# Kernel optimization log

Hardware: AMD Instinct MI355X
Metric: run time of the kernel (lower is better)

## Reference

```python
import jax, jax.numpy as jnp
import numpy as np

N_FILTER = 64
IMAGE_SIZE = 64
CHANNELS = 3
N_CALLS = 16  # n_calls * 16 with n_calls=1
EPS = 1e-5


def _sobel_kernels(c):
    kx = jnp.array([[-1., 0., 1.], [-2., 0., 2.], [-1., 0., 1.]], jnp.float32) / 8.0
    ky = kx.T
    # depthwise OIHW kernels: (C, 1, 3, 3)
    return jnp.tile(kx[None, None], (c, 1, 1, 1)), jnp.tile(ky[None, None], (c, 1, 1, 1))


def _dwconv(x, k):
    return jax.lax.conv_general_dilated(
        x, k, window_strides=(1, 1), padding='SAME',
        feature_group_count=x.shape[1],
        dimension_numbers=('NCHW', 'OIHW', 'NCHW'))


def setup_inputs() -> dict:
    key = jax.random.key(0)
    k1, k2, k3 = jax.random.split(key, 3)
    B, L = 16, 512
    fin, fout = N_FILTER * 3, N_FILTER
    return {
        'lat': jax.random.normal(k1, (B, L), jnp.float32),
        'Wk': jax.random.normal(k2, (L, fin * fout), jnp.float32) * 0.02,
        'bk': jnp.zeros((fin * fout,), jnp.float32),
        'Wb': jax.random.normal(k3, (L, fout), jnp.float32) * 0.02,
        'bb': jnp.zeros((fout,), jnp.float32),
        'leak_factor': jnp.asarray(0.1, jnp.float32),
    }


def reference(lat, Wk, bk, Wb, bb, leak_factor):
    B = lat.shape[0]
    fin, fout = N_FILTER * 3, N_FILTER
    kx, ky = _sobel_kernels(N_FILTER)

    # seed: zeros with a 1.0 in channel 0 at the image center
    out0 = jnp.zeros((B, N_FILTER, IMAGE_SIZE, IMAGE_SIZE), jnp.float32)
    out0 = out0.at[:, 0, IMAGE_SIZE // 2, IMAGE_SIZE // 2].set(1.0)

    leak = jnp.clip(leak_factor, 0.001, 1000.0)

    # per-sample dynamic 1x1 conv weights/bias (constant across the loop)
    w = (lat @ Wk + bk).reshape(B, fout, fin)   # (B, fout, fin)
    b = (lat @ Wb + bb)                          # (B, fout)

    def step(out, _):
        # Sobel perception: [identity, grad_x, grad_y] -> (B, 3*nf, H, W)
        p = jnp.concatenate([out, _dwconv(out, kx), _dwconv(out, ky)], axis=1)
        # InstanceNorm2d (affine=False): normalize over H, W per sample/channel
        mu = p.mean(axis=(2, 3), keepdims=True)
        var = p.var(axis=(2, 3), keepdims=True)
        p = (p - mu) * jax.lax.rsqrt(var + EPS)
        # latent-conditioned dynamic 1x1 conv
        new = jnp.einsum('bchw,boc->bohw', p, w) + b[:, :, None, None]
        out = out + leak * new
        return out, out

    out, embs = jax.lax.scan(step, out0, None, length=N_CALLS)
    out_embs = jnp.concatenate([out0[None], embs], axis=0)  # (N_CALLS+1, B, nf, H, W)

    out_raw = out[:, :CHANNELS]
    return jnp.clip(out_raw, -1.0, 1.0), out_embs, out_raw
```

## Files before the change

kernel.cpp:

```cpp
#include <hip/hip_runtime.h>
#include <cstdint>
#include <cstddef>

#define NB 16
#define NC 64
#define HW 4096
#define SLICE ((size_t)(NB*NC*HW))
#define NSTEP 16

#define WS_WT    ((size_t)0)
#define WS_BV    ((size_t)196608)
#define WS_SV    ((size_t)197632)
#define WS_SVMU  ((size_t)200704)
#define WS_PLA   ((size_t)203776)
#define WS_PLB   ((size_t)4398080)

typedef _Float16 half8 __attribute__((ext_vector_type(8)));
typedef float f32x4 __attribute__((ext_vector_type(4)));

__global__ __launch_bounds__(256) void k_w(const float* __restrict__ lat,
    const float* __restrict__ Wk, const float* __restrict__ bk,
    const float* __restrict__ Wb, const float* __restrict__ bb,
    float* __restrict__ wT, float* __restrict__ bvec) {
  int t = threadIdx.x;
  if (blockIdx.x < 48) {
    int j = blockIdx.x*256 + t;
    float acc[16];
#pragma unroll
    for (int b = 0; b < 16; b++) acc[b] = 0.f;
#pragma unroll 4
    for (int k = 0; k < 512; k++) {
      float wv = Wk[(size_t)k*12288 + j];
#pragma unroll
      for (int b = 0; b < 16; b++) acc[b] = fmaf(lat[b*512 + k], wv, acc[b]);
    }
    int o = j / 192, cf = j % 192;
    int g = cf >> 6, c = cf & 63;
    float bkj = bk[j];
#pragma unroll
    for (int b = 0; b < 16; b++)
      wT[(((size_t)(b*3 + g))*64 + o)*64 + c] = acc[b] + bkj;
  } else if (t < 64) {
    int j = t;
    float acc[16];
#pragma unroll
    for (int b = 0; b < 16; b++) acc[b] = 0.f;
    for (int k = 0; k < 512; k++) {
      float wv = Wb[k*64 + j];
#pragma unroll
      for (int b = 0; b < 16; b++) acc[b] = fmaf(lat[b*512 + k], wv, acc[b]);
    }
    float bbj = bb[j];
#pragma unroll
    for (int b = 0; b < 16; b++) bvec[b*64 + j] = acc[b] + bbj;
  }
}

__global__ void k_init(float* __restrict__ e0, float* __restrict__ plA) {
  int f4 = blockIdx.x*256 + threadIdx.x;
  float4 v = make_float4(0.f, 0.f, 0.f, 0.f);
  if (f4 < 1048576) {
    if ((f4 & 65535) == 520) v.x = 1.0f;
    *(float4*)(e0 + (size_t)f4*4) = v;
  } else {
    int g4 = f4 - 1048576;
    if ((g4 & 65535) == 2080)
      v.x = __uint_as_float(0x00003C00u);
    *(float4*)(plA + (size_t)g4*4) = v;
  }
}

__global__ __launch_bounds__(256) void k_stats(const float* __restrict__ st,
    float* __restrict__ svb, float* __restrict__ svmub) {
  int c = blockIdx.x, b = blockIdx.y, t = threadIdx.x;
  __shared__ float red[4][6];
  const float* base = st + (size_t)(b*NC + c) * HW;
  int w = t & 63, wv = t >> 6, h0 = wv * 16;
  float x[18];
#pragma unroll
  for (int i = 0; i < 18; i++) {
    int row = h0 - 1 + i;
    x[i] = (row >= 0 && row < 64) ? base[row*64 + w] : 0.f;
  }
  float d[18], s[18];
#pragma unroll
  for (int i = 0; i < 18; i++) {
    float xl = __shfl(x[i], (w + 63) & 63);
    float xr = __shfl(x[i], (w + 1) & 63);
    if (w == 0)  xl = 0.f;
    if (w == 63) xr = 0.f;
    d[i] = xr - xl; s[i] = xl + 2.f*x[i] + xr;
  }
  float s0=0,q0=0,s1=0,q1=0,s2=0,q2=0;
#pragma unroll
  for (int k = 0; k < 16; k++) {
    float v  = x[k+1];
    float gx = (d[k] + 2.f*d[k+1] + d[k+2]) * 0.125f;
    float gy = (s[k+2] - s[k]) * 0.125f;
    s0 += v;  q0 = fmaf(v, v, q0);
    s1 += gx; q1 = fmaf(gx, gx, q1);
    s2 += gy; q2 = fmaf(gy, gy, q2);
  }
#pragma unroll
  for (int off = 32; off >= 1; off >>= 1) {
    s0 += __shfl_xor(s0, off); q0 += __shfl_xor(q0, off);
    s1 += __shfl_xor(s1, off); q1 += __shfl_xor(q1, off);
    s2 += __shfl_xor(s2, off); q2 += __shfl_xor(q2, off);
  }
  int lane = t & 63;
  if (lane == 0) {
    red[wv][0]=s0; red[wv][1]=q0; red[wv][2]=s1;
    red[wv][3]=q1; red[wv][4]=s2; red[wv][5]=q2;
  }
  __syncthreads();
  if (t == 0) {
    float r[6];
#pragma unroll
    for (int u = 0; u < 6; u++) r[u] = red[0][u]+red[1][u]+red[2][u]+red[3][u];
#pragma unroll
    for (int g = 0; g < 3; g++) {
      float mu  = r[2*g] * (1.f/HW);
      float var = fmaxf(r[2*g+1]*(1.f/HW) - mu*mu, 0.f);
      float sv  = 1.f / sqrtf(var + 1e-5f);
      svb  [b*192 + g*64 + c] = sv;
      svmub[b*192 + g*64 + c] = sv * mu;
    }
  }
}

struct SG {
  alignas(16) _Float16 Bwin[32768];
  float biasL[64];
};

__global__ __launch_bounds__(256, 2) void k_gemm(const float* __restrict__ st,
    float* __restrict__ stn, const float* __restrict__ wT,
    const float* __restrict__ bvec, const float* __restrict__ svb,
    const float* __restrict__ svmub, const _Float16* __restrict__ plR,
    _Float16* __restrict__ plW, const float* __restrict__ leakp,
    float* __restrict__ out0, float* __restrict__ out2, int last) {
  __shared__ SG sh;
  int bid = blockIdx.x, t = threadIdx.x;
  int b = bid >> 5;
  int r0 = ((((bid & 7) << 2) | ((bid >> 3) & 3))) << 1;
  int lane = t & 63, wt = t >> 6, c4 = lane >> 4;
  float leak = fminf(fmaxf(leakp[0], 0.001f), 1000.f);

  const _Float16* plb = plR + (size_t)b*524288;
#pragma unroll
  for (int i = 0; i < 16; i++) {
    int u = t + i*256;
    int pl = u >> 11, rest = u & 2047;
    int pxg = (r0 - 1)*64 + (rest & 255);
    int pxc = pxg < 0 ? 0 : (pxg > 4095 ? 4095 : pxg);
    const _Float16* gp = plb + ((size_t)pl*8 + (rest >> 8))*32768 + (size_t)pxc*8;
    float4 v = *(const float4*)gp;
    if (pxg < 0 || pxg > 4095) v = make_float4(0.f,0.f,0.f,0.f);
    *(float4*)(sh.Bwin + (size_t)u*8) = v;
  }

  int oa = wt*16 + (lane & 15);
  half8 whi[3][2], wlo[3][2];
  float biasacc = 0.f;
#pragma unroll
  for (int g = 0; g < 3; g++) {
#pragma unroll
    for (int kc = 0; kc < 2; kc++) {
      const float* wrow = wT + (((size_t)(b*3 + g))*64 + oa)*64 + kc*32 + c4*8;
      const float* svp  = svb   + b*192 + g*64 + kc*32 + c4*8;
      const float* svmp = svmub + b*192 + g*64 + kc*32 + c4*8;
      float4 wa = *(const float4*)wrow;  float4 wb2 = *(const float4*)(wrow + 4);
      float4 sa = *(const float4*)svp;   float4 sb2 = *(const float4*)(svp + 4);
      float4 ma = *(const float4*)svmp;  float4 mb2 = *(const float4*)(svmp + 4);
      float wv[8] = {wa.x,wa.y,wa.z,wa.w, wb2.x,wb2.y,wb2.z,wb2.w};
      float sv[8] = {sa.x,sa.y,sa.z,sa.w, sb2.x,sb2.y,sb2.z,sb2.w};
      float mv[8] = {ma.x,ma.y,ma.z,ma.w, mb2.x,mb2.y,mb2.z,mb2.w};
      half8 hv, lv;
#pragma unroll
      for (int jj = 0; jj < 8; jj++) {
        float scaled = wv[jj] * sv[jj];
        biasacc = fmaf(wv[jj], mv[jj], biasacc);
        _Float16 h = (_Float16)scaled;
        hv[jj] = h;
        lv[jj] = (_Float16)(scaled - (float)h);
      }
      whi[g][kc] = hv; wlo[g][kc] = lv;
    }
  }
  biasacc += __shfl_xor(biasacc, 16);
  biasacc += __shfl_xor(biasacc, 32);
  if (c4 == 0) sh.biasL[oa] = bvec[b*64 + oa] - biasacc;
  __syncthreads();

#pragma unroll
  for (int rr = 0; rr < 2; rr++) {
    int r = r0 + rr;
    f32x4 accA[4] = {}; f32x4 accB[12] = {}; f32x4 accC[12] = {};
#pragma unroll
    for (int kc = 0; kc < 2; kc++) {
#pragma unroll
      for (int n = 0; n < 12; n++) {
        int pxl = rr*64 + n*16 + (lane & 15);
        half8 bh = *(const half8*)(sh.Bwin + ((size_t)(     kc*4 + c4)*256 + pxl)*8);
        half8 bl = *(const half8*)(sh.Bwin + ((size_t)(8 +  kc*4 + c4)*256 + pxl)*8);
        accB[n] = __builtin_amdgcn_mfma_f32_16x16x32_f16(whi[1][kc], bh, accB[n], 0,0,0);
        accB[n] = __builtin_amdgcn_mfma_f32_16x16x32_f16(whi[1][kc], bl, accB[n], 0,0,0);
        accB[n] = __builtin_amdgcn_mfma_f32_16x16x32_f16(wlo[1][kc], bh, accB[n], 0,0,0);
        accC[n] = __builtin_amdgcn_mfma_f32_16x16x32_f16(whi[2][kc], bh, accC[n], 0,0,0);
        accC[n] = __builtin_amdgcn_mfma_f32_16x16x32_f16(whi[2][kc], bl, accC[n], 0,0,0);
        accC[n] = __builtin_amdgcn_mfma_f32_16x16x32_f16(wlo[2][kc], bh, accC[n], 0,0,0);
        if (n >= 4 && n < 8) {
          accA[n-4] = __builtin_amdgcn_mfma_f32_16x16x32_f16(whi[0][kc], bh, accA[n-4], 0,0,0);
          accA[n-4] = __builtin_amdgcn_mfma_f32_16x16x32_f16(whi[0][kc], bl, accA[n-4], 0,0,0);
          accA[n-4] = __builtin_amdgcn_mfma_f32_16x16x32_f16(wlo[0][kc], bh, accA[n-4], 0,0,0);
        }
      }
    }

    float nv16[16];
#pragma unroll
    for (int j = 0; j < 4; j++) {
      int o = wt*16 + (c4 << 2) + j;
      float Sx[4], Sy[4];
#pragma unroll
      for (int nc = 0; nc < 4; nc++) {
        Sx[nc] = accB[nc][j] + 2.f*accB[4+nc][j] + accB[8+nc][j];
        Sy[nc] = accC[8+nc][j] - accC[nc][j];
      }
      float bt = sh.biasL[o];
#pragma unroll
      for (int nc = 0; nc < 4; nc++) {
        int nm = (nc > 0) ? nc-1 : 0;
        int np = (nc < 3) ? nc+1 : 3;
        float xl1 = __shfl(Sx[nc], (lane - 1) & 63);
        float xl2 = (nc > 0) ? __shfl(Sx[nm], (lane + 15) & 63) : 0.f;
        float xL  = (lane & 15) ? xl1 : xl2;
        float xr1 = __shfl(Sx[nc], (lane + 1) & 63);
        float xr2 = (nc < 3) ? __shfl(Sx[np], (lane - 15) & 63) : 0.f;
        float xR  = ((lane & 15) == 15) ? xr2 : xr1;
        float yl1 = __shfl(Sy[nc], (lane - 1) & 63);
        float yl2 = (nc > 0) ? __shfl(Sy[nm], (lane + 15) & 63) : 0.f;
        float yL  = (lane & 15) ? yl1 : yl2;
        float yr1 = __shfl(Sy[nc], (lane + 1) & 63);
        float yr2 = (nc < 3) ? __shfl(Sy[np], (lane - 15) & 63) : 0.f;
        float yR  = ((lane & 15) == 15) ? yr2 : yr1;
        float gx = (xR - xL) * 0.125f;
        float gy = (yL + 2.f*Sy[nc] + yR) * 0.125f;
        float nw = accA[nc][j] + gx + gy + bt;
        int wpx = nc*16 + (lane & 15);
        size_t gi = (size_t)(b*NC + o)*HW + (size_t)r*64 + wpx;
        float nvv = st[gi] + leak * nw;
        stn[gi] = nvv;
        nv16[j*4 + nc] = nvv;
        if (last && o < 3) {
          size_t oi = (size_t)(b*3 + o)*HW + (size_t)r*64 + wpx;
          out2[oi] = nvv;
          out0[oi] = fminf(fmaxf(nvv, -1.f), 1.f);
        }
      }
    }

    if (!last) {
      int pl = c4 & 1;
      int g8 = wt*2 + (c4 >> 1);
      _Float16* pw = plW + (size_t)b*524288 + ((size_t)pl*8 + g8)*32768;
#pragma unroll
      for (int nc = 0; nc < 4; nc++) {
        float own[4], rcv[4];
#pragma unroll
        for (int j = 0; j < 4; j++) {
          own[j] = nv16[j*4 + nc];
          rcv[j] = __shfl_xor(own[j], 16);
        }
        float xx[8];
#pragma unroll
        for (int jj = 0; jj < 8; jj++)
          xx[jj] = ((jj >> 2) == (c4 & 1)) ? own[jj & 3] : rcv[jj & 3];
        half8 v8;
        if (pl == 0) {
#pragma unroll
          for (int jj = 0; jj < 8; jj++) v8[jj] = (_Float16)xx[jj];
        } else {
#pragma unroll
          for (int jj = 0; jj < 8; jj++) {
            _Float16 h = (_Float16)xx[jj];
            v8[jj] = (_Float16)(xx[jj] - (float)h);
          }
        }
        int gpx = r*64 + nc*16 + (lane & 15);
        *(half8*)(pw + (size_t)gpx*8) = v8;
      }
    }
  }
}

extern "C" void kernel_launch(void* const* d_in, const int* in_sizes, int n_in,
                              void* d_out, int out_size, void* d_ws, size_t ws_size,
                              hipStream_t stream) {
  const float* lat   = (const float*)d_in[0];
  const float* Wk    = (const float*)d_in[1];
  const float* bk    = (const float*)d_in[2];
  const float* Wb    = (const float*)d_in[3];
  const float* bb    = (const float*)d_in[4];
  const float* leakp = (const float*)d_in[5];
  float* out = (float*)d_out;
  float* ws  = (float*)d_ws;
  float* wT    = ws + WS_WT;
  float* bvec  = ws + WS_BV;
  float* svbuf = ws + WS_SV;
  float* svmub = ws + WS_SVMU;
  _Float16* plbuf[2] = { (_Float16*)(ws + WS_PLA), (_Float16*)(ws + WS_PLB) };
  float* out0 = out;
  float* embs = out + 196608;
  float* out2 = out + 196608 + 17*SLICE;

  hipLaunchKernelGGL(k_w,    dim3(49),   dim3(256), 0, stream, lat, Wk, bk, Wb, bb, wT, bvec);
  hipLaunchKernelGGL(k_init, dim3(8192), dim3(256), 0, stream, embs, ws + WS_PLA);
  for (int tstep = 0; tstep < NSTEP; tstep++) {
    const float* stc = embs + (size_t)tstep*SLICE;
    float*       stn = embs + (size_t)(tstep+1)*SLICE;
    hipLaunchKernelGGL(k_stats, dim3(64,16), dim3(256), 0, stream, stc, svbuf, svmub);
    hipLaunchKernelGGL(k_gemm, dim3(512), dim3(256), 0, stream,
                       stc, stn, wT, bvec, svbuf, svmub,
                       plbuf[tstep & 1], plbuf[(tstep+1) & 1], leakp,
                       out0, out2, (int)(tstep == NSTEP-1));
  }
}
```

Baseline: 600.4 us.

## Fuse instance-norm statistics into step kernel via halo recompute and atomics

Removes the separate per-step statistics kernel: each step kernel now recomputes one halo row above and below its two output rows so it can compute Sobel gradients of the new state and accumulate sum and sum-of-squares per channel with atomics into a triple-buffered stats array. The next step turns these sums into scale and shift in shared memory. This saves 16 kernel launches and a full re-read of the state each step. In exchange it doubles the MFMA work per block (4 rows instead of 2), enlarges shared memory, drops to one block per CU, and adds atomic contention.

```diff
diff --git a/kernel.cpp b/kernel.cpp
--- a/kernel.cpp
+++ b/kernel.cpp
@@ -10,10 +10,9 @@
 
 #define WS_WT    ((size_t)0)
 #define WS_BV    ((size_t)196608)
-#define WS_SV    ((size_t)197632)
-#define WS_SVMU  ((size_t)200704)
-#define WS_PLA   ((size_t)203776)
-#define WS_PLB   ((size_t)4398080)
+#define WS_STATS ((size_t)197632)
+#define WS_PLA   ((size_t)216064)
+#define WS_PLB   ((size_t)4410368)
 
 typedef _Float16 half8 __attribute__((ext_vector_type(8)));
 typedef float f32x4 __attribute__((ext_vector_type(4)));
@@ -56,8 +55,21 @@
   }
 }
 
-__global__ void k_init(float* __restrict__ e0, float* __restrict__ plA) {
-  int f4 = blockIdx.x*256 + threadIdx.x;
+__global__ void k_init(float* __restrict__ e0, float* __restrict__ plA,
+                       float* __restrict__ sb0, float* __restrict__ sb1) {
+  int t = threadIdx.x;
+  if (blockIdx.x == 0) {
+    for (int i = t; i < 6144; i += 256) {
+      int rem = i % 384;
+      int gc = rem >> 1, e = rem & 1;
+      float v = 0.f;
+      if (gc == 0) v = 1.0f;
+      else if ((gc == 64 || gc == 128) && e == 1) v = 0.1875f;
+      sb0[i] = v;
+      sb1[i] = 0.f;
+    }
+  }
+  int f4 = blockIdx.x*256 + t;
   float4 v = make_float4(0.f, 0.f, 0.f, 0.f);
   if (f4 < 1048576) {
     if ((f4 & 65535) == 520) v.x = 1.0f;
@@ -70,94 +82,48 @@
   }
 }
 
-__global__ __launch_bounds__(256) void k_stats(const float* __restrict__ st,
-    float* __restrict__ svb, float* __restrict__ svmub) {
-  int c = blockIdx.x, b = blockIdx.y, t = threadIdx.x;
-  __shared__ float red[4][6];
-  const float* base = st + (size_t)(b*NC + c) * HW;
-  int w = t & 63, wv = t >> 6, h0 = wv * 16;
-  float x[18];
-#pragma unroll
-  for (int i = 0; i < 18; i++) {
-    int row = h0 - 1 + i;
-    x[i] = (row >= 0 && row < 64) ? base[row*64 + w] : 0.f;
-  }
-  float d[18], s[18];
-#pragma unroll
-  for (int i = 0; i < 18; i++) {
-    float xl = __shfl(x[i], (w + 63) & 63);
-    float xr = __shfl(x[i], (w + 1) & 63);
-    if (w == 0)  xl = 0.f;
-    if (w == 63) xr = 0.f;
-    d[i] = xr - xl; s[i] = xl + 2.f*x[i] + xr;
-  }
-  float s0=0,q0=0,s1=0,q1=0,s2=0,q2=0;
-#pragma unroll
-  for (int k = 0; k < 16; k++) {
-    float v  = x[k+1];
-    float gx = (d[k] + 2.f*d[k+1] + d[k+2]) * 0.125f;
-    float gy = (s[k+2] - s[k]) * 0.125f;
-    s0 += v;  q0 = fmaf(v, v, q0);
-    s1 += gx; q1 = fmaf(gx, gx, q1);
-    s2 += gy; q2 = fmaf(gy, gy, q2);
-  }
-#pragma unroll
-  for (int off = 32; off >= 1; off >>= 1) {
-    s0 += __shfl_xor(s0, off); q0 += __shfl_xor(q0, off);
-    s1 += __shfl_xor(s1, off); q1 += __shfl_xor(q1, off);
-    s2 += __shfl_xor(s2, off); q2 += __shfl_xor(q2, off);
-  }
-  int lane = t & 63;
-  if (lane == 0) {
-    red[wv][0]=s0; red[wv][1]=q0; red[wv][2]=s1;
-    red[wv][3]=q1; red[wv][4]=s2; red[wv][5]=q2;
-  }
-  __syncthreads();
-  if (t == 0) {
-    float r[6];
-#pragma unroll
-    for (int u = 0; u < 6; u++) r[u] = red[0][u]+red[1][u]+red[2][u]+red[3][u];
-#pragma unroll
-    for (int g = 0; g < 3; g++) {
-      float mu  = r[2*g] * (1.f/HW);
-      float var = fmaxf(r[2*g+1]*(1.f/HW) - mu*mu, 0.f);
-      float sv  = 1.f / sqrtf(var + 1e-5f);
-      svb  [b*192 + g*64 + c] = sv;
-      svmub[b*192 + g*64 + c] = sv * mu;
-    }
-  }
-}
-
-struct SG {
-  alignas(16) _Float16 Bwin[32768];
-  float biasL[64];
+struct SG2 {
+  alignas(16) _Float16 Bwin[16*384*8];
+  float svL[192], svmuL[192], biasL[64];
 };
 
-__global__ __launch_bounds__(256, 2) void k_gemm(const float* __restrict__ st,
+__global__ __launch_bounds__(256, 1) void k_step(const float* __restrict__ st,
     float* __restrict__ stn, const float* __restrict__ wT,
-    const float* __restrict__ bvec, const float* __restrict__ svb,
-    const float* __restrict__ svmub, const _Float16* __restrict__ plR,
-    _Float16* __restrict__ plW, const float* __restrict__ leakp,
+    const float* __restrict__ bvec, const float* __restrict__ statsR,
+    float* __restrict__ statsW, float* __restrict__ statsZ,
+    const _Float16* __restrict__ plR, _Float16* __restrict__ plW,
+    const float* __restrict__ leakp,
     float* __restrict__ out0, float* __restrict__ out2, int last) {
-  __shared__ SG sh;
+  __shared__ SG2 sh;
   int bid = blockIdx.x, t = threadIdx.x;
   int b = bid >> 5;
   int r0 = ((((bid & 7) << 2) | ((bid >> 3) & 3))) << 1;
   int lane = t & 63, wt = t >> 6, c4 = lane >> 4;
   float leak = fminf(fmaxf(leakp[0], 0.001f), 1000.f);
 
+  if (t < 12) statsZ[bid*12 + t] = 0.f;
+
   const _Float16* plb = plR + (size_t)b*524288;
 #pragma unroll
-  for (int i = 0; i < 16; i++) {
+  for (int i = 0; i < 24; i++) {
     int u = t + i*256;
-    int pl = u >> 11, rest = u & 2047;
-    int pxg = (r0 - 1)*64 + (rest & 255);
+    int p = u / 384, wpx = u % 384;
+    int pxg = (r0 - 2)*64 + wpx;
     int pxc = pxg < 0 ? 0 : (pxg > 4095 ? 4095 : pxg);
-    const _Float16* gp = plb + ((size_t)pl*8 + (rest >> 8))*32768 + (size_t)pxc*8;
-    float4 v = *(const float4*)gp;
+    float4 v = *(const float4*)(plb + ((size_t)p*4096 + pxc)*8);
     if (pxg < 0 || pxg > 4095) v = make_float4(0.f,0.f,0.f,0.f);
-    *(float4*)(sh.Bwin + (size_t)u*8) = v;
-  }
+    *(float4*)(sh.Bwin + ((size_t)p*384 + wpx)*8) = v;
+  }
+
+  if (t < 192) {
+    float s = statsR[(b*192 + t)*2];
+    float q = statsR[(b*192 + t)*2 + 1];
+    float mu = s * (1.f/HW);
+    float var = fmaxf(q*(1.f/HW) - mu*mu, 0.f);
+    float sv = 1.f / sqrtf(var + 1e-5f);
+    sh.svL[t] = sv; sh.svmuL[t] = sv * mu;
+  }
+  __syncthreads();
 
   int oa = wt*16 + (lane & 15);
   half8 whi[3][2], wlo[3][2];
@@ -167,19 +133,14 @@
 #pragma unroll
     for (int kc = 0; kc < 2; kc++) {
       const float* wrow = wT + (((size_t)(b*3 + g))*64 + oa)*64 + kc*32 + c4*8;
-      const float* svp  = svb   + b*192 + g*64 + kc*32 + c4*8;
-      const float* svmp = svmub + b*192 + g*64 + kc*32 + c4*8;
       float4 wa = *(const float4*)wrow;  float4 wb2 = *(const float4*)(wrow + 4);
-      float4 sa = *(const float4*)svp;   float4 sb2 = *(const float4*)(svp + 4);
-      float4 ma = *(const float4*)svmp;  float4 mb2 = *(const float4*)(svmp + 4);
       float wv[8] = {wa.x,wa.y,wa.z,wa.w, wb2.x,wb2.y,wb2.z,wb2.w};
-      float sv[8] = {sa.x,sa.y,sa.z,sa.w, sb2.x,sb2.y,sb2.z,sb2.w};
-      float mv[8] = {ma.x,ma.y,ma.z,ma.w, mb2.x,mb2.y,mb2.z,mb2.w};
       half8 hv, lv;
 #pragma unroll
       for (int jj = 0; jj < 8; jj++) {
-        float scaled = wv[jj] * sv[jj];
-        biasacc = fmaf(wv[jj], mv[jj], biasacc);
+        int cg = g*64 + kc*32 + c4*8 + jj;
+        float scaled = wv[jj] * sh.svL[cg];
+        biasacc = fmaf(wv[jj], sh.svmuL[cg], biasacc);
         _Float16 h = (_Float16)scaled;
         hv[jj] = h;
         lv[jj] = (_Float16)(scaled - (float)h);
@@ -192,75 +153,87 @@
   if (c4 == 0) sh.biasL[oa] = bvec[b*64 + oa] - biasacc;
   __syncthreads();
 
-#pragma unroll
-  for (int rr = 0; rr < 2; rr++) {
-    int r = r0 + rr;
-    f32x4 accA[4] = {}; f32x4 accB[12] = {}; f32x4 accC[12] = {};
-#pragma unroll
-    for (int kc = 0; kc < 2; kc++) {
-#pragma unroll
-      for (int n = 0; n < 12; n++) {
-        int pxl = rr*64 + n*16 + (lane & 15);
-        half8 bh = *(const half8*)(sh.Bwin + ((size_t)(     kc*4 + c4)*256 + pxl)*8);
-        half8 bl = *(const half8*)(sh.Bwin + ((size_t)(8 +  kc*4 + c4)*256 + pxl)*8);
-        accB[n] = __builtin_amdgcn_mfma_f32_16x16x32_f16(whi[1][kc], bh, accB[n], 0,0,0);
-        accB[n] = __builtin_amdgcn_mfma_f32_16x16x32_f16(whi[1][kc], bl, accB[n], 0,0,0);
-        accB[n] = __builtin_amdgcn_mfma_f32_16x16x32_f16(wlo[1][kc], bh, accB[n], 0,0,0);
-        accC[n] = __builtin_amdgcn_mfma_f32_16x16x32_f16(whi[2][kc], bh, accC[n], 0,0,0);
-        accC[n] = __builtin_amdgcn_mfma_f32_16x16x32_f16(whi[2][kc], bl, accC[n], 0,0,0);
-        accC[n] = __builtin_amdgcn_mfma_f32_16x16x32_f16(wlo[2][kc], bh, accC[n], 0,0,0);
-        if (n >= 4 && n < 8) {
-          accA[n-4] = __builtin_amdgcn_mfma_f32_16x16x32_f16(whi[0][kc], bh, accA[n-4], 0,0,0);
-          accA[n-4] = __builtin_amdgcn_mfma_f32_16x16x32_f16(whi[0][kc], bl, accA[n-4], 0,0,0);
-          accA[n-4] = __builtin_amdgcn_mfma_f32_16x16x32_f16(wlo[0][kc], bh, accA[n-4], 0,0,0);
-        }
-      }
-    }
-
-    float nv16[16];
-#pragma unroll
-    for (int j = 0; j < 4; j++) {
-      int o = wt*16 + (c4 << 2) + j;
-      float Sx[4], Sy[4];
-#pragma unroll
-      for (int nc = 0; nc < 4; nc++) {
-        Sx[nc] = accB[nc][j] + 2.f*accB[4+nc][j] + accB[8+nc][j];
-        Sy[nc] = accC[8+nc][j] - accC[nc][j];
-      }
-      float bt = sh.biasL[o];
-#pragma unroll
-      for (int nc = 0; nc < 4; nc++) {
-        int nm = (nc > 0) ? nc-1 : 0;
-        int np = (nc < 3) ? nc+1 : 3;
-        float xl1 = __shfl(Sx[nc], (lane - 1) & 63);
-        float xl2 = (nc > 0) ? __shfl(Sx[nm], (lane + 15) & 63) : 0.f;
-        float xL  = (lane & 15) ? xl1 : xl2;
-        float xr1 = __shfl(Sx[nc], (lane + 1) & 63);
-        float xr2 = (nc < 3) ? __shfl(Sx[np], (lane - 15) & 63) : 0.f;
-        float xR  = ((lane & 15) == 15) ? xr2 : xr1;
-        float yl1 = __shfl(Sy[nc], (lane - 1) & 63);
-        float yl2 = (nc > 0) ? __shfl(Sy[nm], (lane + 15) & 63) : 0.f;
-        float yL  = (lane & 15) ? yl1 : yl2;
-        float yr1 = __shfl(Sy[nc], (lane + 1) & 63);
-        float yr2 = (nc < 3) ? __shfl(Sy[np], (lane - 15) & 63) : 0.f;
-        float yR  = ((lane & 15) == 15) ? yr2 : yr1;
-        float gx = (xR - xL) * 0.125f;
-        float gy = (yL + 2.f*Sy[nc] + yR) * 0.125f;
-        float nw = accA[nc][j] + gx + gy + bt;
-        int wpx = nc*16 + (lane & 15);
-        size_t gi = (size_t)(b*NC + o)*HW + (size_t)r*64 + wpx;
-        float nvv = st[gi] + leak * nw;
-        stn[gi] = nvv;
-        nv16[j*4 + nc] = nvv;
-        if (last && o < 3) {
-          size_t oi = (size_t)(b*3 + o)*HW + (size_t)r*64 + wpx;
-          out2[oi] = nvv;
-          out0[oi] = fminf(fmaxf(nvv, -1.f), 1.f);
-        }
-      }
-    }
-
-    if (!last) {
+  float nv4[4][16];
+
+#pragma unroll
+  for (int rr = 0; rr < 4; rr++) {
+    int r = r0 - 1 + rr;
+    if (r >= 0 && r < 64) {
+      f32x4 accA[4] = {}; f32x4 accB[12] = {}; f32x4 accC[12] = {};
+#pragma unroll
+      for (int kc = 0; kc < 2; kc++) {
+#pragma unroll
+        for (int n = 0; n < 12; n++) {
+          int pxl = rr*64 + n*16 + (lane & 15);
+          half8 bh = *(const half8*)(sh.Bwin + ((size_t)((     kc*4 + c4)*384) + pxl)*8);
+          half8 bl = *(const half8*)(sh.Bwin + ((size_t)((8 +  kc*4 + c4)*384) + pxl)*8);
+          accB[n] = __builtin_amdgcn_mfma_f32_16x16x32_f16(whi[1][kc], bh, accB[n], 0,0,0);
+          accB[n] = __builtin_amdgcn_mfma_f32_16x16x32_f16(whi[1][kc], bl, accB[n], 0,0,0);
+          accB[n] = __builtin_amdgcn_mfma_f32_16x16x32_f16(wlo[1][kc], bh, accB[n], 0,0,0);
+          accC[n] = __builtin_amdgcn_mfma_f32_16x16x32_f16(whi[2][kc], bh, accC[n], 0,0,0);
+          accC[n] = __builtin_amdgcn_mfma_f32_16x16x32_f16(whi[2][kc], bl, accC[n], 0,0,0);
+          accC[n] = __builtin_amdgcn_mfma_f32_16x16x32_f16(wlo[2][kc], bh, accC[n], 0,0,0);
+          if (n >= 4 && n < 8) {
+            accA[n-4] = __builtin_amdgcn_mfma_f32_16x16x32_f16(whi[0][kc], bh, accA[n-4], 0,0,0);
+            accA[n-4] = __builtin_amdgcn_mfma_f32_16x16x32_f16(whi[0][kc], bl, accA[n-4], 0,0,0);
+            accA[n-4] = __builtin_amdgcn_mfma_f32_16x16x32_f16(wlo[0][kc], bh, accA[n-4], 0,0,0);
+          }
+        }
+      }
+
+#pragma unroll
+      for (int j = 0; j < 4; j++) {
+        int o = wt*16 + (c4 << 2) + j;
+        float Sx[4], Sy[4];
+#pragma unroll
+        for (int nc = 0; nc < 4; nc++) {
+          Sx[nc] = accB[nc][j] + 2.f*accB[4+nc][j] + accB[8+nc][j];
+          Sy[nc] = accC[8+nc][j] - accC[nc][j];
+        }
+        float bt = sh.biasL[o];
+#pragma unroll
+        for (int nc = 0; nc < 4; nc++) {
+          int nm = (nc > 0) ? nc-1 : 0;
+          int np = (nc < 3) ? nc+1 : 3;
+          float xl1 = __shfl(Sx[nc], (lane - 1) & 63);
+          float xl2 = (nc > 0) ? __shfl(Sx[nm], (lane + 15) & 63) : 0.f;
+          float xL  = (lane & 15) ? xl1 : xl2;
+          float xr1 = __shfl(Sx[nc], (lane + 1) & 63);
+          float xr2 = (nc < 3) ? __shfl(Sx[np], (lane - 15) & 63) : 0.f;
+          float xR  = ((lane & 15) == 15) ? xr2 : xr1;
+          float yl1 = __shfl(Sy[nc], (lane - 1) & 63);
+          float yl2 = (nc > 0) ? __shfl(Sy[nm], (lane + 15) & 63) : 0.f;
+          float yL  = (lane & 15) ? yl1 : yl2;
+          float yr1 = __shfl(Sy[nc], (lane + 1) & 63);
+          float yr2 = (nc < 3) ? __shfl(Sy[np], (lane - 15) & 63) : 0.f;
+          float yR  = ((lane & 15) == 15) ? yr2 : yr1;
+          float gx = (xR - xL) * 0.125f;
+          float gy = (yL + 2.f*Sy[nc] + yR) * 0.125f;
+          float nw = accA[nc][j] + gx + gy + bt;
+          int wpx = nc*16 + (lane & 15);
+          size_t gi = (size_t)(b*NC + o)*HW + (size_t)r*64 + wpx;
+          float nvv = st[gi] + leak * nw;
+          nv4[rr][j*4 + nc] = nvv;
+          if (rr == 1 || rr == 2) {
+            stn[gi] = nvv;
+            if (last && o < 3) {
+              size_t oi = (size_t)(b*3 + o)*HW + (size_t)r*64 + wpx;
+              out2[oi] = nvv;
+              out0[oi] = fminf(fmaxf(nvv, -1.f), 1.f);
+            }
+          }
+        }
+      }
+    } else {
+#pragma unroll
+      for (int u = 0; u < 16; u++) nv4[rr][u] = 0.f;
+    }
+  }
+
+  if (!last) {
+#pragma unroll
+    for (int rr = 1; rr <= 2; rr++) {
+      int r = r0 - 1 + rr;
       int pl = c4 & 1;
       int g8 = wt*2 + (c4 >> 1);
       _Float16* pw = plW + (size_t)b*524288 + ((size_t)pl*8 + g8)*32768;
@@ -269,7 +242,7 @@
         float own[4], rcv[4];
 #pragma unroll
         for (int j = 0; j < 4; j++) {
-          own[j] = nv16[j*4 + nc];
+          own[j] = nv4[rr][j*4 + nc];
           rcv[j] = __shfl_xor(own[j], 16);
         }
         float xx[8];
@@ -289,6 +262,58 @@
         }
         int gpx = r*64 + nc*16 + (lane & 15);
         *(half8*)(pw + (size_t)gpx*8) = v8;
+      }
+    }
+
+#pragma unroll
+    for (int j = 0; j < 4; j++) {
+      float dxv[4][4], sxv[4][4];
+#pragma unroll
+      for (int rw = 0; rw < 4; rw++) {
+        float vv[4];
+#pragma unroll
+        for (int nc = 0; nc < 4; nc++) vv[nc] = nv4[rw][j*4 + nc];
+#pragma unroll
+        for (int nc = 0; nc < 4; nc++) {
+          int nm = (nc > 0) ? nc-1 : 0;
+          int np = (nc < 3) ? nc+1 : 3;
+          float xl1 = __shfl(vv[nc], (lane - 1) & 63);
+          float xl2 = (nc > 0) ? __shfl(vv[nm], (lane + 15) & 63) : 0.f;
+          float xL  = (lane & 15) ? xl1 : xl2;
+          float xr1 = __shfl(vv[nc], (lane + 1) & 63);
+          float xr2 = (nc < 3) ? __shfl(vv[np], (lane - 15) & 63) : 0.f;
+          float xR  = ((lane & 15) == 15) ? xr2 : xr1;
+          dxv[rw][nc] = xR - xL;
+          sxv[rw][nc] = xL + 2.f*vv[nc] + xR;
+        }
+      }
+      float s0=0,q0=0,s1=0,q1=0,s2=0,q2=0;
+#pragma unroll
+      for (int rr = 1; rr <= 2; rr++) {
+#pragma unroll
+        for (int nc = 0; nc < 4; nc++) {
+          float v = nv4[rr][j*4 + nc];
+          s0 += v; q0 = fmaf(v, v, q0);
+          float gx = (dxv[rr-1][nc] + 2.f*dxv[rr][nc] + dxv[rr+1][nc]) * 0.125f;
+          float gy = (sxv[rr+1][nc] - sxv[rr-1][nc]) * 0.125f;
+          s1 += gx; q1 = fmaf(gx, gx, q1);
+          s2 += gy; q2 = fmaf(gy, gy, q2);
+        }
+      }
+#pragma unroll
+      for (int m = 1; m <= 8; m <<= 1) {
+        s0 += __shfl_xor(s0, m); q0 += __shfl_xor(q0, m);
+        s1 += __shfl_xor(s1, m); q1 += __shfl_xor(q1, m);
+        s2 += __shfl_xor(s2, m); q2 += __shfl_xor(q2, m);
+      }
+      if ((lane & 15) == 0) {
+        int o = wt*16 + (c4 << 2) + j;
+        atomicAdd(&statsW[((size_t)b*192 +       o)*2    ], s0);
+        atomicAdd(&statsW[((size_t)b*192 +       o)*2 + 1], q0);
+        atomicAdd(&statsW[((size_t)b*192 +  64 + o)*2    ], s1);
+        atomicAdd(&statsW[((size_t)b*192 +  64 + o)*2 + 1], q1);
+        atomicAdd(&statsW[((size_t)b*192 + 128 + o)*2    ], s2);
+        atomicAdd(&statsW[((size_t)b*192 + 128 + o)*2 + 1], q2);
       }
     }
   }
@@ -307,21 +332,21 @@
   float* ws  = (float*)d_ws;
   float* wT    = ws + WS_WT;
   float* bvec  = ws + WS_BV;
-  float* svbuf = ws + WS_SV;
-  float* svmub = ws + WS_SVMU;
+  float* sbuf[3] = { ws + WS_STATS, ws + WS_STATS + 6144, ws + WS_STATS + 12288 };
   _Float16* plbuf[2] = { (_Float16*)(ws + WS_PLA), (_Float16*)(ws + WS_PLB) };
   float* out0 = out;
   float* embs = out + 196608;
   float* out2 = out + 196608 + 17*SLICE;
 
   hipLaunchKernelGGL(k_w,    dim3(49),   dim3(256), 0, stream, lat, Wk, bk, Wb, bb, wT, bvec);
-  hipLaunchKernelGGL(k_init, dim3(8192), dim3(256), 0, stream, embs, ws + WS_PLA);
+  hipLaunchKernelGGL(k_init, dim3(8192), dim3(256), 0, stream, embs, ws + WS_PLA,
+                     sbuf[0], sbuf[1]);
   for (int tstep = 0; tstep < NSTEP; tstep++) {
     const float* stc = embs + (size_t)tstep*SLICE;
     float*       stn = embs + (size_t)(tstep+1)*SLICE;
-    hipLaunchKernelGGL(k_stats, dim3(64,16), dim3(256), 0, stream, stc, svbuf, svmub);
-    hipLaunchKernelGGL(k_gemm, dim3(512), dim3(256), 0, stream,
-                       stc, stn, wT, bvec, svbuf, svmub,
+    hipLaunchKernelGGL(k_step, dim3(512), dim3(256), 0, stream,
+                       stc, stn, wT, bvec,
+                       sbuf[tstep % 3], sbuf[(tstep+1) % 3], sbuf[(tstep+2) % 3],
                        plbuf[tstep & 1], plbuf[(tstep+1) & 1], leakp,
                        out0, out2, (int)(tstep == NSTEP-1));
   }
```

Result: slower. 960.3 us (+59.9%).

## Vectorize stats loads and read state from LDS hi/lo halves in gemm

Applied to the files above, without the earlier changes.

The stats kernel now has each thread load float4 row segments (16 threads per row, 4 rows each) instead of scalar per-column loads, with shuffles only at the segment edges. The gemm kernel no longer reads the fp32 previous state from global memory. It reconstructs it from the fp16 hi/lo split planes already staged in shared memory. This removes one full-state global read per step, but the residual update now depends on hi+lo fp16 reconstruction precision and on the LDS window layout matching.

```diff
diff --git a/kernel.cpp b/kernel.cpp
--- a/kernel.cpp
+++ b/kernel.cpp
@@ -75,31 +75,40 @@
   int c = blockIdx.x, b = blockIdx.y, t = threadIdx.x;
   __shared__ float red[4][6];
   const float* base = st + (size_t)(b*NC + c) * HW;
-  int w = t & 63, wv = t >> 6, h0 = wv * 16;
-  float x[18];
-#pragma unroll
-  for (int i = 0; i < 18; i++) {
+  int lane = t & 63;
+  int cg = t & 15;
+  int h0 = (t >> 4) * 4;
+  float4 x4[6];
+#pragma unroll
+  for (int i = 0; i < 6; i++) {
     int row = h0 - 1 + i;
-    x[i] = (row >= 0 && row < 64) ? base[row*64 + w] : 0.f;
-  }
-  float d[18], s[18];
-#pragma unroll
-  for (int i = 0; i < 18; i++) {
-    float xl = __shfl(x[i], (w + 63) & 63);
-    float xr = __shfl(x[i], (w + 1) & 63);
-    if (w == 0)  xl = 0.f;
-    if (w == 63) xr = 0.f;
-    d[i] = xr - xl; s[i] = xl + 2.f*x[i] + xr;
+    if (row >= 0 && row < 64) x4[i] = *(const float4*)(base + row*64 + cg*4);
+    else                      x4[i] = make_float4(0.f,0.f,0.f,0.f);
+  }
+  float d[6][4], s[6][4];
+#pragma unroll
+  for (int i = 0; i < 6; i++) {
+    float xm = __shfl(x4[i].w, (lane + 63) & 63);
+    float xp = __shfl(x4[i].x, (lane + 1) & 63);
+    if (cg == 0)  xm = 0.f;
+    if (cg == 15) xp = 0.f;
+    d[i][0] = x4[i].y - xm;      s[i][0] = xm + 2.f*x4[i].x + x4[i].y;
+    d[i][1] = x4[i].z - x4[i].x; s[i][1] = x4[i].x + 2.f*x4[i].y + x4[i].z;
+    d[i][2] = x4[i].w - x4[i].y; s[i][2] = x4[i].y + 2.f*x4[i].z + x4[i].w;
+    d[i][3] = xp - x4[i].z;      s[i][3] = x4[i].z + 2.f*x4[i].w + xp;
   }
   float s0=0,q0=0,s1=0,q1=0,s2=0,q2=0;
 #pragma unroll
-  for (int k = 0; k < 16; k++) {
-    float v  = x[k+1];
-    float gx = (d[k] + 2.f*d[k+1] + d[k+2]) * 0.125f;
-    float gy = (s[k+2] - s[k]) * 0.125f;
-    s0 += v;  q0 = fmaf(v, v, q0);
-    s1 += gx; q1 = fmaf(gx, gx, q1);
-    s2 += gy; q2 = fmaf(gy, gy, q2);
+  for (int k = 0; k < 4; k++) {
+    float vv[4] = {x4[k+1].x, x4[k+1].y, x4[k+1].z, x4[k+1].w};
+#pragma unroll
+    for (int j = 0; j < 4; j++) {
+      float gx = (d[k][j] + 2.f*d[k+1][j] + d[k+2][j]) * 0.125f;
+      float gy = (s[k+2][j] - s[k][j]) * 0.125f;
+      s0 += vv[j]; q0 = fmaf(vv[j], vv[j], q0);
+      s1 += gx;    q1 = fmaf(gx, gx, q1);
+      s2 += gy;    q2 = fmaf(gy, gy, q2);
+    }
   }
 #pragma unroll
   for (int off = 32; off >= 1; off >>= 1) {
@@ -107,7 +116,7 @@
     s1 += __shfl_xor(s1, off); q1 += __shfl_xor(q1, off);
     s2 += __shfl_xor(s2, off); q2 += __shfl_xor(q2, off);
   }
-  int lane = t & 63;
+  int wv = t >> 6;
   if (lane == 0) {
     red[wv][0]=s0; red[wv][1]=q0; red[wv][2]=s1;
     red[wv][3]=q1; red[wv][4]=s2; red[wv][5]=q2;
@@ -133,7 +142,7 @@
   float biasL[64];
 };
 
-__global__ __launch_bounds__(256, 2) void k_gemm(const float* __restrict__ st,
+__global__ __launch_bounds__(256, 2) void k_gemm(
     float* __restrict__ stn, const float* __restrict__ wT,
     const float* __restrict__ bvec, const float* __restrict__ svb,
     const float* __restrict__ svmub, const _Float16* __restrict__ plR,
@@ -221,6 +230,7 @@
 #pragma unroll
     for (int j = 0; j < 4; j++) {
       int o = wt*16 + (c4 << 2) + j;
+      int c8o = o >> 3, cjo = o & 7;
       float Sx[4], Sy[4];
 #pragma unroll
       for (int nc = 0; nc < 4; nc++) {
@@ -247,13 +257,16 @@
         float gx = (xR - xL) * 0.125f;
         float gy = (yL + 2.f*Sy[nc] + yR) * 0.125f;
         float nw = accA[nc][j] + gx + gy + bt;
-        int wpx = nc*16 + (lane & 15);
-        size_t gi = (size_t)(b*NC + o)*HW + (size_t)r*64 + wpx;
-        float nvv = st[gi] + leak * nw;
+        int wpxc = nc*16 + (lane & 15);
+        int wpx = (1 + rr)*64 + wpxc;
+        float sthi = (float)sh.Bwin[((size_t)c8o*256 + wpx)*8 + cjo];
+        float stlo = (float)sh.Bwin[((size_t)(8 + c8o)*256 + wpx)*8 + cjo];
+        float nvv = sthi + stlo + leak * nw;
+        size_t gi = (size_t)(b*NC + o)*HW + (size_t)r*64 + wpxc;
         stn[gi] = nvv;
         nv16[j*4 + nc] = nvv;
         if (last && o < 3) {
-          size_t oi = (size_t)(b*3 + o)*HW + (size_t)r*64 + wpx;
+          size_t oi = (size_t)(b*3 + o)*HW + (size_t)r*64 + wpxc;
           out2[oi] = nvv;
           out0[oi] = fminf(fmaxf(nvv, -1.f), 1.f);
         }
@@ -321,7 +334,7 @@
     float*       stn = embs + (size_t)(tstep+1)*SLICE;
     hipLaunchKernelGGL(k_stats, dim3(64,16), dim3(256), 0, stream, stc, svbuf, svmub);
     hipLaunchKernelGGL(k_gemm, dim3(512), dim3(256), 0, stream,
-                       stc, stn, wT, bvec, svbuf, svmub,
+                       stn, wT, bvec, svbuf, svmub,
                        plbuf[tstep & 1], plbuf[(tstep+1) & 1], leakp,
                        out0, out2, (int)(tstep == NSTEP-1));
   }
```

New measurement: 585.7 us, median of 2. 1.03x faster.
